# Kernel optimization log

Measured on AMD Instinct MI355X. Metric: run time of the kernel, lower is better.

The kernel has to match this reference:

```python
import jax, jax.numpy as jnp
import numpy as np
from math import sqrt

DIM = 256

def setup_inputs() -> dict:
    key = jax.random.key(0)
    k1, k2, k3, k4 = jax.random.split(key, 4)
    B, T, D, H, R = 2, 4096, DIM, 8, 32
    # xavier-uniform-ish scaled params
    def xavier(k, shape, fan_in, fan_out):
        a = sqrt(6.0 / (fan_in + fan_out))
        return jax.random.uniform(k, shape, jnp.float32, -a, a)
    x = jax.random.normal(k1, (B, T, D), jnp.float32)
    Q = xavier(k2, (H, R, D), D, R)
    K = xavier(k3, (H, R, D), D, R)
    VO = xavier(k4, (H, D, D), D, D)
    return {"x": x, "Q": Q, "K": K, "VO": VO}

def reference(x, Q, K, VO):
    # x: [b,t,d]; Q,K: [h,r,d]; VO: [h,d,e]
    d = x.shape[-1]
    q = jnp.einsum('btd,hrd->bhtr', x, Q)          # low-rank query proj
    k = jnp.einsum('bud,hrd->bhur', x, K)          # low-rank key proj
    scores = jnp.einsum('bhtr,bhur->bhtu', q, k) / sqrt(d)
    attn = jax.nn.softmax(scores, axis=-1)         # softmax over u (keys)
    ctx = jnp.einsum('bhtu,bud->bhtd', attn, x)    # values are raw x
    out = jnp.einsum('bhtd,hde->bte', ctx, VO)     # fused value-output proj, summed over heads
    return out
```

## Files before the change

### kernel.cpp

```cpp
#include <hip/hip_runtime.h>
#include <hip/hip_bf16.h>
#include <cstdint>
#include <cstddef>

typedef __attribute__((ext_vector_type(8))) __bf16 bf16x8;
typedef __attribute__((ext_vector_type(4))) float f32x4;
typedef __attribute__((ext_vector_type(16))) float f32x16;

#define MFMA16(a, b, c) __builtin_amdgcn_mfma_f32_16x16x32_bf16((a), (b), (c), 0, 0, 0)
#define MFMA32(a, b, c) __builtin_amdgcn_mfma_f32_32x32x16_bf16((a), (b), (c), 0, 0, 0)

__device__ __forceinline__ f32x16 zf16() {
    f32x16 z;
    #pragma unroll
    for (int r = 0; r < 16; ++r) z[r] = 0.f;
    return z;
}

__device__ __forceinline__ unsigned pk2(float lo, float hi) {
    unsigned w;
    asm("v_cvt_pk_bf16_f32 %0, %1, %2" : "=v"(w) : "v"(lo), "v"(hi));
    return w;
}
__device__ __forceinline__ void swap32(unsigned& a, unsigned& b) {
    asm("v_permlane32_swap_b32 %0, %1" : "+v"(a), "+v"(b));
}
__device__ __forceinline__ bf16x8 mkfrag(unsigned a, unsigned b, unsigned c, unsigned d) {
    union { unsigned u[4]; bf16x8 v; } x;
    x.u[0] = a; x.u[1] = b; x.u[2] = c; x.u[3] = d;
    return x.v;
}

__global__ __launch_bounds__(256) void prep(const float* __restrict__ x,
                                            const float* __restrict__ Qw,
                                            const float* __restrict__ Kw,
                                            const float* __restrict__ VO,
                                            __bf16* __restrict__ xT,
                                            __bf16* __restrict__ xrow,
                                            __bf16* __restrict__ wb,
                                            __bf16* __restrict__ vot) {
    __shared__ float tile[64][65];
    const int bid = blockIdx.x;
    if (bid < 512) {
        const int b = bid >> 8;
        const int rem = bid & 255;
        const int tt = rem >> 2, dd = rem & 3;
        const int t0 = tt * 64, d0 = dd * 64;
        #pragma unroll
        for (int j = 0; j < 16; ++j) {
            int idx = j * 256 + threadIdx.x;
            int t = idx >> 6, d = idx & 63;
            float v = x[((size_t)(b * 4096 + t0 + t)) * 256 + d0 + d];
            tile[t][d] = v;
            xrow[((size_t)(b * 4096 + t0 + t)) * 256 + d0 + d] = (__bf16)v;
        }
        __syncthreads();
        #pragma unroll
        for (int j = 0; j < 16; ++j) {
            int idx = j * 256 + threadIdx.x;
            int d = idx >> 6, t = idx & 63;
            xT[((size_t)(b * 256 + d0 + d)) * 4096 + t0 + t] = (__bf16)tile[t][d];
        }
    } else if (bid < 640) {
        const int k = bid - 512;
        const int h = k >> 4;
        const int rem = k & 15;
        const int dt = rem >> 2, et = rem & 3;
        const int d0 = dt * 64, e0 = et * 64;
        #pragma unroll
        for (int j = 0; j < 16; ++j) {
            int idx = j * 256 + threadIdx.x;
            int d = idx >> 6, e = idx & 63;
            tile[d][e] = VO[((size_t)(h * 256 + d0 + d)) * 256 + e0 + e];
        }
        __syncthreads();
        #pragma unroll
        for (int j = 0; j < 16; ++j) {
            int idx = j * 256 + threadIdx.x;
            int e = idx >> 6, d = idx & 63;
            vot[((size_t)(e0 + e)) * 2048 + h * 256 + d0 + d] = (__bf16)tile[d][e];
        }
    } else {
        const float cl = 1.4426950408889634f / 16.0f;
        #pragma unroll
        for (int e = 0; e < 2; ++e) {
            int i = (bid - 640) * 512 + e * 256 + threadIdx.x;
            float v = (i < 65536) ? Qw[i] * cl : Kw[i - 65536];
            wb[i] = (__bf16)v;
        }
    }
}

__global__ __launch_bounds__(256) void proj_kernel(const __bf16* __restrict__ xrow,
                                                   const __bf16* __restrict__ wb,
                                                   __bf16* __restrict__ qo,
                                                   __bf16* __restrict__ ko) {
    const int w = threadIdx.x >> 6;
    const int l = threadIdx.x & 63;
    const int g = l >> 4, c = l & 15;
    const int tg = blockIdx.x * 64 + w * 16;

    bf16x8 af[8];
    #pragma unroll
    for (int kk = 0; kk < 8; ++kk)
        af[kk] = *(const bf16x8*)(xrow + (size_t)(tg + c) * 256 + kk * 32 + g * 8);

    const int b = tg >> 12, t = tg & 4095;
    #pragma unroll
    for (int hs = 0; hs < 16; ++hs) {
        const int h = hs >> 1, s = hs & 1;
        const __bf16* W = wb + (size_t)(s * 8 + h) * 8192;
        f32x4 acc0 = {0.f, 0.f, 0.f, 0.f}, acc1 = {0.f, 0.f, 0.f, 0.f};
        #pragma unroll
        for (int kk = 0; kk < 8; ++kk) {
            bf16x8 b0 = *(const bf16x8*)(W + (size_t)c * 256 + kk * 32 + g * 8);
            bf16x8 b1 = *(const bf16x8*)(W + (size_t)(16 + c) * 256 + kk * 32 + g * 8);
            acc0 = MFMA16(af[kk], b0, acc0);
            acc1 = MFMA16(af[kk], b1, acc1);
        }
        __bf16* outp = s ? ko : qo;
        const size_t obase = (size_t)(b * 8 + h) * 4096 + t;
        #pragma unroll
        for (int i = 0; i < 4; ++i) {
            outp[(obase + 4 * g + i) * 32 + c]      = (__bf16)acc0[i];
            outp[(obase + 4 * g + i) * 32 + 16 + c] = (__bf16)acc1[i];
        }
    }
}

__device__ __forceinline__ void stage_x(const __bf16* __restrict__ xTg_b,
                                        unsigned char* xbuf, int u0, int tid) {
    #pragma unroll
    for (int j = 0; j < 4; ++j) {
        int ch = j * 512 + tid;
        int d = ch >> 3;
        int slog = (ch & 7) ^ (d & 7);
        const __bf16* src = xTg_b + (size_t)d * 4096 + u0 + slog * 8;
        unsigned char* dst = xbuf + (size_t)(j * 512 + (tid & ~63)) * 16;
        __builtin_amdgcn_global_load_lds(
            (const __attribute__((address_space(1))) unsigned int*)src,
            (__attribute__((address_space(3))) unsigned int*)dst, 16, 0, 0);
    }
}

#define MKFRAG(dst, V, base)                                   \
    {                                                          \
        unsigned wa = pk2(V[(base) + 0], V[(base) + 1]);       \
        unsigned wb_ = pk2(V[(base) + 2], V[(base) + 3]);      \
        unsigned wc = pk2(V[(base) + 4], V[(base) + 5]);       \
        unsigned wd = pk2(V[(base) + 6], V[(base) + 7]);       \
        swap32(wa, wc);                                        \
        swap32(wb_, wd);                                       \
        dst = mkfrag(wa, wb_, wc, wd);                         \
    }

__global__ __launch_bounds__(512, 2) void attn_kernel(const __bf16* __restrict__ qg,
                                                      const __bf16* __restrict__ kg,
                                                      const __bf16* __restrict__ xTg,
                                                      __bf16* __restrict__ ctx) {
    __shared__ __align__(16) unsigned char lds[65536 + 1024];
    unsigned char* xbuf0 = lds;
    unsigned char* xbuf1 = lds + 32768;

    const int bid = blockIdx.x;
    const int bh = bid >> 4;
    const int tt = bid & 15;
    const int b = bh >> 3, h = bh & 7;
    const int t0 = tt * 256;
    const int tid = threadIdx.x;
    const int w = tid >> 6;
    const int l = tid & 63;
    const int l31 = l & 31, hi = l >> 5;

    float* scale_w = (float*)(lds + 65536) + w * 32;

    const __bf16* xTg_b = xTg + (size_t)b * 256 * 4096;
    const __bf16* kg_bh = kg + (size_t)bh * 4096 * 32;

    const size_t qoff = ((size_t)bh * 4096 + t0 + w * 32 + l31) * 32;
    const bf16x8 qf0 = *(const bf16x8*)(qg + qoff + hi * 8);
    const bf16x8 qf1 = *(const bf16x8*)(qg + qoff + 16 + hi * 8);

    f32x16 acc[8];
    #pragma unroll
    for (int n = 0; n < 8; ++n)
        #pragma unroll
        for (int r = 0; r < 16; ++r) acc[n][r] = 0.f;

    float lsum = 0.f;
    const int swz = (l31 & 7) << 4;

    bf16x8 kA[2][2];
    #pragma unroll
    for (int s = 0; s < 2; ++s)
        #pragma unroll
        for (int st = 0; st < 2; ++st)
            kA[s][st] = *(const bf16x8*)(kg_bh + (size_t)(s * 32 + l31) * 32 + st * 16 + hi * 8);

    stage_x(xTg_b, xbuf0, 0, tid);
    __syncthreads();

    bf16x8 pf[4];
    for (int ut = 0; ut < 64; ++ut) {
        unsigned char* xcur = (ut & 1) ? xbuf1 : xbuf0;
        unsigned char* xnxt = (ut & 1) ? xbuf0 : xbuf1;
        if (ut < 63) stage_x(xTg_b, xnxt, (ut + 1) * 64, tid);

        f32x16 s0 = MFMA32(kA[0][0], qf0, zf16());
        s0 = MFMA32(kA[0][1], qf1, s0);
        f32x16 s1 = MFMA32(kA[1][0], qf0, zf16());
        s1 = MFMA32(kA[1][1], qf1, s1);

        if (ut < 63) {
            const __bf16* kp = kg_bh + (size_t)(ut + 1) * 64 * 32;
            #pragma unroll
            for (int s = 0; s < 2; ++s)
                #pragma unroll
                for (int st = 0; st < 2; ++st)
                    kA[s][st] = *(const bf16x8*)(kp + (size_t)(s * 32 + l31) * 32 + st * 16 + hi * 8);
        }

        float rs = 0.f;
        #pragma unroll
        for (int r = 0; r < 16; ++r) {
            float p = __builtin_amdgcn_exp2f(s0[r]);
            s0[r] = p; rs += p;
        }
        #pragma unroll
        for (int r = 0; r < 16; ++r) {
            float p = __builtin_amdgcn_exp2f(s1[r]);
            s1[r] = p; rs += p;
        }
        lsum += rs;

        bf16x8 pf0, pf1, pf2, pf3;
        MKFRAG(pf0, s0, 0);
        MKFRAG(pf1, s0, 8);
        MKFRAG(pf2, s1, 0);
        MKFRAG(pf3, s1, 8);
        pf[0] = pf0; pf[1] = pf1; pf[2] = pf2; pf[3] = pf3;

        __builtin_amdgcn_s_setprio(1);
        #pragma unroll
        for (int kk = 0; kk < 4; ++kk) {
            #pragma unroll
            for (int n = 0; n < 8; ++n) {
                const bf16x8 xb = *(const bf16x8*)(xcur + (n * 32 + l31) * 128 +
                                                   ((kk * 32 + hi * 16) ^ swz));
                acc[n] = MFMA32(pf[kk], xb, acc[n]);
            }
        }
        __builtin_amdgcn_s_setprio(0);

        asm volatile("s_waitcnt vmcnt(4)" ::: "memory");
        __builtin_amdgcn_s_barrier();
    }

    lsum += __shfl_xor(lsum, 32);
    const float linv = 1.0f / lsum;
    if (!hi) scale_w[l31] = linv;
    f32x4 iv[4];
    #pragma unroll
    for (int q4 = 0; q4 < 4; ++q4)
        iv[q4] = *(const f32x4*)&scale_w[q4 * 8 + hi * 4];
    #pragma unroll
    for (int n = 0; n < 8; ++n) {
        #pragma unroll
        for (int r = 0; r < 16; ++r) {
            int t = t0 + w * 32 + (r & 3) + 8 * (r >> 2) + 4 * hi;
            int d = n * 32 + l31;
            ctx[((size_t)(b * 4096 + t) * 8 + h) * 256 + d] =
                (__bf16)(acc[n][r] * iv[r >> 2][r & 3]);
        }
    }
}

__global__ __launch_bounds__(256) void gemm_out(const __bf16* __restrict__ ctx,
                                                const __bf16* __restrict__ vot,
                                                float* __restrict__ out) {
    const int bid = blockIdx.x;
    const int mt2 = bid >> 1;
    const int eh = bid & 1;
    const int w = threadIdx.x >> 6;
    const int l = threadIdx.x & 63;
    const int l31 = l & 31, hi = l >> 5;
    const size_t a0row = (size_t)(mt2 * 64 + l31) * 2048;
    const size_t a1row = (size_t)(mt2 * 64 + 32 + l31) * 2048;
    const size_t brow  = (size_t)(eh * 128 + w * 32 + l31) * 2048;
    f32x16 acc0 = zf16(), acc1 = zf16();
    #pragma unroll 4
    for (int kk = 0; kk < 128; ++kk) {
        bf16x8 bfr = *(const bf16x8*)(vot + brow + kk * 16 + hi * 8);
        bf16x8 a0  = *(const bf16x8*)(ctx + a0row + kk * 16 + hi * 8);
        bf16x8 a1  = *(const bf16x8*)(ctx + a1row + kk * 16 + hi * 8);
        acc0 = MFMA32(a0, bfr, acc0);
        acc1 = MFMA32(a1, bfr, acc1);
    }
    const int e = eh * 128 + w * 32 + l31;
    #pragma unroll
    for (int r = 0; r < 16; ++r) {
        int crow = (r & 3) + 8 * (r >> 2) + 4 * hi;
        out[(size_t)(mt2 * 64 + crow) * 256 + e]      = acc0[r];
        out[(size_t)(mt2 * 64 + 32 + crow) * 256 + e] = acc1[r];
    }
}

extern "C" void kernel_launch(void* const* d_in, const int* in_sizes, int n_in,
                              void* d_out, int out_size, void* d_ws, size_t ws_size,
                              hipStream_t stream) {
    const float* x  = (const float*)d_in[0];
    const float* Qw = (const float*)d_in[1];
    const float* Kw = (const float*)d_in[2];
    const float* VO = (const float*)d_in[3];
    float* out = (float*)d_out;

    char* ws = (char*)d_ws;
    __bf16* xT   = (__bf16*)(ws);
    __bf16* xrow = (__bf16*)(ws + ((size_t)4 << 20));
    __bf16* qb   = (__bf16*)(ws + ((size_t)8 << 20));
    __bf16* kb   = (__bf16*)(ws + ((size_t)12 << 20));
    __bf16* wb   = (__bf16*)(ws + ((size_t)16 << 20));
    __bf16* vot  = (__bf16*)(ws + ((size_t)17 << 20));
    __bf16* ctx  = (__bf16*)(ws + ((size_t)18 << 20));

    prep<<<896, 256, 0, stream>>>(x, Qw, Kw, VO, xT, xrow, wb, vot);
    proj_kernel<<<128, 256, 0, stream>>>(xrow, wb, qb, kb);
    attn_kernel<<<256, 512, 0, stream>>>(qb, kb, xT, ctx);
    gemm_out<<<256, 256, 0, stream>>>(ctx, vot, out);
}
```

Baseline: 242.9 us.

## Split attention warps into 64-query by 128-dim tiles to halve LDS reads

Each warp now owns 64 queries and half of the 256 value dimensions, where before it owned 32 queries and all 256 dimensions. Every x fragment read from LDS now feeds two MFMAs (one per 32-query half), which halves LDS read traffic per MFMA in the PV product. The cost is that each warp computes twice as many QK scores and exponentials, so QK^T and exp work is duplicated across the two warps sharing a query group. Register use per warp stays about the same.

```diff
diff --git a/kernel.cpp b/kernel.cpp
--- a/kernel.cpp
+++ b/kernel.cpp
@@ -158,7 +158,7 @@
                                                       const __bf16* __restrict__ kg,
                                                       const __bf16* __restrict__ xTg,
                                                       __bf16* __restrict__ ctx) {
-    __shared__ __align__(16) unsigned char lds[65536 + 1024];
+    __shared__ __align__(16) unsigned char lds[65536 + 2048];
     unsigned char* xbuf0 = lds;
     unsigned char* xbuf1 = lds + 32768;
 
@@ -169,25 +169,32 @@
     const int t0 = tt * 256;
     const int tid = threadIdx.x;
     const int w = tid >> 6;
+    const int qgi = w >> 1;
+    const int dh = w & 1;
     const int l = tid & 63;
     const int l31 = l & 31, hi = l >> 5;
 
-    float* scale_w = (float*)(lds + 65536) + w * 32;
+    float* scale_w = (float*)(lds + 65536) + w * 64;
 
     const __bf16* xTg_b = xTg + (size_t)b * 256 * 4096;
     const __bf16* kg_bh = kg + (size_t)bh * 4096 * 32;
 
-    const size_t qoff = ((size_t)bh * 4096 + t0 + w * 32 + l31) * 32;
-    const bf16x8 qf0 = *(const bf16x8*)(qg + qoff + hi * 8);
-    const bf16x8 qf1 = *(const bf16x8*)(qg + qoff + 16 + hi * 8);
-
-    f32x16 acc[8];
-    #pragma unroll
-    for (int n = 0; n < 8; ++n)
-        #pragma unroll
-        for (int r = 0; r < 16; ++r) acc[n][r] = 0.f;
-
-    float lsum = 0.f;
+    bf16x8 qf[2][2];
+    #pragma unroll
+    for (int qh = 0; qh < 2; ++qh) {
+        const size_t qoff = ((size_t)bh * 4096 + t0 + qgi * 64 + qh * 32 + l31) * 32;
+        qf[qh][0] = *(const bf16x8*)(qg + qoff + hi * 8);
+        qf[qh][1] = *(const bf16x8*)(qg + qoff + 16 + hi * 8);
+    }
+
+    f32x16 acc[2][4];
+    #pragma unroll
+    for (int qh = 0; qh < 2; ++qh)
+        #pragma unroll
+        for (int n = 0; n < 4; ++n)
+            acc[qh][n] = zf16();
+
+    float lsum0 = 0.f, lsum1 = 0.f;
     const int swz = (l31 & 7) << 4;
 
     bf16x8 kA[2][2];
@@ -200,16 +207,19 @@
     stage_x(xTg_b, xbuf0, 0, tid);
     __syncthreads();
 
-    bf16x8 pf[4];
     for (int ut = 0; ut < 64; ++ut) {
         unsigned char* xcur = (ut & 1) ? xbuf1 : xbuf0;
         unsigned char* xnxt = (ut & 1) ? xbuf0 : xbuf1;
         if (ut < 63) stage_x(xTg_b, xnxt, (ut + 1) * 64, tid);
 
-        f32x16 s0 = MFMA32(kA[0][0], qf0, zf16());
-        s0 = MFMA32(kA[0][1], qf1, s0);
-        f32x16 s1 = MFMA32(kA[1][0], qf0, zf16());
-        s1 = MFMA32(kA[1][1], qf1, s1);
+        f32x16 s00 = MFMA32(kA[0][0], qf[0][0], zf16());
+        s00 = MFMA32(kA[0][1], qf[0][1], s00);
+        f32x16 s01 = MFMA32(kA[1][0], qf[0][0], zf16());
+        s01 = MFMA32(kA[1][1], qf[0][1], s01);
+        f32x16 s10 = MFMA32(kA[0][0], qf[1][0], zf16());
+        s10 = MFMA32(kA[0][1], qf[1][1], s10);
+        f32x16 s11 = MFMA32(kA[1][0], qf[1][0], zf16());
+        s11 = MFMA32(kA[1][1], qf[1][1], s11);
 
         if (ut < 63) {
             const __bf16* kp = kg_bh + (size_t)(ut + 1) * 64 * 32;
@@ -220,34 +230,37 @@
                     kA[s][st] = *(const bf16x8*)(kp + (size_t)(s * 32 + l31) * 32 + st * 16 + hi * 8);
         }
 
-        float rs = 0.f;
+        float rs0 = 0.f, rs1 = 0.f;
         #pragma unroll
         for (int r = 0; r < 16; ++r) {
-            float p = __builtin_amdgcn_exp2f(s0[r]);
-            s0[r] = p; rs += p;
-        }
-        #pragma unroll
-        for (int r = 0; r < 16; ++r) {
-            float p = __builtin_amdgcn_exp2f(s1[r]);
-            s1[r] = p; rs += p;
-        }
-        lsum += rs;
-
-        bf16x8 pf0, pf1, pf2, pf3;
-        MKFRAG(pf0, s0, 0);
-        MKFRAG(pf1, s0, 8);
-        MKFRAG(pf2, s1, 0);
-        MKFRAG(pf3, s1, 8);
-        pf[0] = pf0; pf[1] = pf1; pf[2] = pf2; pf[3] = pf3;
+            float p;
+            p = __builtin_amdgcn_exp2f(s00[r]); s00[r] = p; rs0 += p;
+            p = __builtin_amdgcn_exp2f(s01[r]); s01[r] = p; rs0 += p;
+            p = __builtin_amdgcn_exp2f(s10[r]); s10[r] = p; rs1 += p;
+            p = __builtin_amdgcn_exp2f(s11[r]); s11[r] = p; rs1 += p;
+        }
+        lsum0 += rs0;
+        lsum1 += rs1;
+
+        bf16x8 pf0[4], pf1[4];
+        MKFRAG(pf0[0], s00, 0);
+        MKFRAG(pf0[1], s00, 8);
+        MKFRAG(pf0[2], s01, 0);
+        MKFRAG(pf0[3], s01, 8);
+        MKFRAG(pf1[0], s10, 0);
+        MKFRAG(pf1[1], s10, 8);
+        MKFRAG(pf1[2], s11, 0);
+        MKFRAG(pf1[3], s11, 8);
 
         __builtin_amdgcn_s_setprio(1);
         #pragma unroll
         for (int kk = 0; kk < 4; ++kk) {
             #pragma unroll
-            for (int n = 0; n < 8; ++n) {
-                const bf16x8 xb = *(const bf16x8*)(xcur + (n * 32 + l31) * 128 +
-                                                   ((kk * 32 + hi * 16) ^ swz));
-                acc[n] = MFMA32(pf[kk], xb, acc[n]);
+            for (int n = 0; n < 4; ++n) {
+                const bf16x8 xb = *(const bf16x8*)(xcur +
+                    (dh * 128 + n * 32 + l31) * 128 + ((kk * 32 + hi * 16) ^ swz));
+                acc[0][n] = MFMA32(pf0[kk], xb, acc[0][n]);
+                acc[1][n] = MFMA32(pf1[kk], xb, acc[1][n]);
             }
         }
         __builtin_amdgcn_s_setprio(0);
@@ -256,21 +269,27 @@
         __builtin_amdgcn_s_barrier();
     }
 
-    lsum += __shfl_xor(lsum, 32);
-    const float linv = 1.0f / lsum;
-    if (!hi) scale_w[l31] = linv;
-    f32x4 iv[4];
-    #pragma unroll
-    for (int q4 = 0; q4 < 4; ++q4)
-        iv[q4] = *(const f32x4*)&scale_w[q4 * 8 + hi * 4];
-    #pragma unroll
-    for (int n = 0; n < 8; ++n) {
-        #pragma unroll
-        for (int r = 0; r < 16; ++r) {
-            int t = t0 + w * 32 + (r & 3) + 8 * (r >> 2) + 4 * hi;
-            int d = n * 32 + l31;
-            ctx[((size_t)(b * 4096 + t) * 8 + h) * 256 + d] =
-                (__bf16)(acc[n][r] * iv[r >> 2][r & 3]);
+    lsum0 += __shfl_xor(lsum0, 32);
+    lsum1 += __shfl_xor(lsum1, 32);
+    if (!hi) {
+        scale_w[l31]      = 1.0f / lsum0;
+        scale_w[32 + l31] = 1.0f / lsum1;
+    }
+    #pragma unroll
+    for (int qh = 0; qh < 2; ++qh) {
+        f32x4 iv[4];
+        #pragma unroll
+        for (int q4 = 0; q4 < 4; ++q4)
+            iv[q4] = *(const f32x4*)&scale_w[qh * 32 + q4 * 8 + hi * 4];
+        #pragma unroll
+        for (int n = 0; n < 4; ++n) {
+            #pragma unroll
+            for (int r = 0; r < 16; ++r) {
+                int t = t0 + qgi * 64 + qh * 32 + (r & 3) + 8 * (r >> 2) + 4 * hi;
+                int d = dh * 128 + n * 32 + l31;
+                ctx[((size_t)(b * 4096 + t) * 8 + h) * 256 + d] =
+                    (__bf16)(acc[qh][n][r] * iv[r >> 2][r & 3]);
+            }
         }
     }
 }
```

Result: slower. 285.0 us (+17.4%).

## Switch attention P·V to FP8 MFMA with FP8-transposed x and register-staged LDS

Applied to the files above, without the earlier changes.

The transposed copy of x is now stored as FP8 instead of bf16, and the softmax probabilities are packed to FP8 so the P·V product uses the 32x32x16 FP8 MFMA. The aim is to halve the bytes of x read per tile and to use the faster FP8 matrix path. The direct global-to-LDS async loads are replaced by register loads written into a padded LDS layout (72-byte rows, no XOR swizzle) followed by a full __syncthreads. This risks accuracy loss from FP8 rounding of both x and the probabilities, and may stall more on the register-staged prefetch.

```diff
diff --git a/kernel.cpp b/kernel.cpp
--- a/kernel.cpp
+++ b/kernel.cpp
@@ -9,6 +9,7 @@
 
 #define MFMA16(a, b, c) __builtin_amdgcn_mfma_f32_16x16x32_bf16((a), (b), (c), 0, 0, 0)
 #define MFMA32(a, b, c) __builtin_amdgcn_mfma_f32_32x32x16_bf16((a), (b), (c), 0, 0, 0)
+#define MFMA8(a, b, c)  __builtin_amdgcn_mfma_f32_32x32x16_fp8_fp8((a), (b), (c), 0, 0, 0)
 
 __device__ __forceinline__ f32x16 zf16() {
     f32x16 z;
@@ -17,25 +18,15 @@
     return z;
 }
 
-__device__ __forceinline__ unsigned pk2(float lo, float hi) {
-    unsigned w;
-    asm("v_cvt_pk_bf16_f32 %0, %1, %2" : "=v"(w) : "v"(lo), "v"(hi));
-    return w;
-}
 __device__ __forceinline__ void swap32(unsigned& a, unsigned& b) {
     asm("v_permlane32_swap_b32 %0, %1" : "+v"(a), "+v"(b));
-}
-__device__ __forceinline__ bf16x8 mkfrag(unsigned a, unsigned b, unsigned c, unsigned d) {
-    union { unsigned u[4]; bf16x8 v; } x;
-    x.u[0] = a; x.u[1] = b; x.u[2] = c; x.u[3] = d;
-    return x.v;
 }
 
 __global__ __launch_bounds__(256) void prep(const float* __restrict__ x,
                                             const float* __restrict__ Qw,
                                             const float* __restrict__ Kw,
                                             const float* __restrict__ VO,
-                                            __bf16* __restrict__ xT,
+                                            unsigned char* __restrict__ x8T,
                                             __bf16* __restrict__ xrow,
                                             __bf16* __restrict__ wb,
                                             __bf16* __restrict__ vot) {
@@ -56,10 +47,14 @@
         }
         __syncthreads();
         #pragma unroll
-        for (int j = 0; j < 16; ++j) {
+        for (int j = 0; j < 8; ++j) {
             int idx = j * 256 + threadIdx.x;
-            int d = idx >> 6, t = idx & 63;
-            xT[((size_t)(b * 256 + d0 + d)) * 4096 + t0 + t] = (__bf16)tile[t][d];
+            int d = idx >> 5, tp = idx & 31;
+            float v0 = tile[tp * 2][d];
+            float v1 = tile[tp * 2 + 1][d];
+            int wpk = __builtin_amdgcn_cvt_pk_fp8_f32(v0, v1, 0, false);
+            *(unsigned short*)(x8T + (size_t)(b * 256 + d0 + d) * 4096 + t0 + tp * 2) =
+                (unsigned short)wpk;
         }
     } else if (bid < 640) {
         const int k = bid - 512;
@@ -128,39 +123,28 @@
     }
 }
 
-__device__ __forceinline__ void stage_x(const __bf16* __restrict__ xTg_b,
-                                        unsigned char* xbuf, int u0, int tid) {
-    #pragma unroll
-    for (int j = 0; j < 4; ++j) {
-        int ch = j * 512 + tid;
-        int d = ch >> 3;
-        int slog = (ch & 7) ^ (d & 7);
-        const __bf16* src = xTg_b + (size_t)d * 4096 + u0 + slog * 8;
-        unsigned char* dst = xbuf + (size_t)(j * 512 + (tid & ~63)) * 16;
-        __builtin_amdgcn_global_load_lds(
-            (const __attribute__((address_space(1))) unsigned int*)src,
-            (__attribute__((address_space(3))) unsigned int*)dst, 16, 0, 0);
-    }
-}
-
-#define MKFRAG(dst, V, base)                                   \
-    {                                                          \
-        unsigned wa = pk2(V[(base) + 0], V[(base) + 1]);       \
-        unsigned wb_ = pk2(V[(base) + 2], V[(base) + 3]);      \
-        unsigned wc = pk2(V[(base) + 4], V[(base) + 5]);       \
-        unsigned wd = pk2(V[(base) + 6], V[(base) + 7]);       \
-        swap32(wa, wc);                                        \
-        swap32(wb_, wd);                                       \
-        dst = mkfrag(wa, wb_, wc, wd);                         \
+
+#define MK8FRAG(dst, V, base)                                                  \
+    {                                                                          \
+        unsigned d0 = 0, d1 = 0;                                               \
+        d0 = __builtin_amdgcn_cvt_pk_fp8_f32(V[(base) + 0], V[(base) + 1], d0, false); \
+        d0 = __builtin_amdgcn_cvt_pk_fp8_f32(V[(base) + 2], V[(base) + 3], d0, true);  \
+        d1 = __builtin_amdgcn_cvt_pk_fp8_f32(V[(base) + 4], V[(base) + 5], d1, false); \
+        d1 = __builtin_amdgcn_cvt_pk_fp8_f32(V[(base) + 6], V[(base) + 7], d1, true);  \
+        swap32(d0, d1);                                                        \
+        union { unsigned u[2]; long l; } z;                                    \
+        z.u[0] = d0; z.u[1] = d1;                                              \
+        dst = z.l;                                                             \
     }
 
 __global__ __launch_bounds__(512, 2) void attn_kernel(const __bf16* __restrict__ qg,
                                                       const __bf16* __restrict__ kg,
-                                                      const __bf16* __restrict__ xTg,
+                                                      const unsigned char* __restrict__ x8g,
                                                       __bf16* __restrict__ ctx) {
-    __shared__ __align__(16) unsigned char lds[65536 + 1024];
+    __shared__ __align__(16) unsigned char lds[2 * 18432 + 1024];
     unsigned char* xbuf0 = lds;
-    unsigned char* xbuf1 = lds + 32768;
+    unsigned char* xbuf1 = lds + 18432;
+    float* scale_base = (float*)(lds + 36864);
 
     const int bid = blockIdx.x;
     const int bh = bid >> 4;
@@ -172,10 +156,13 @@
     const int l = tid & 63;
     const int l31 = l & 31, hi = l >> 5;
 
-    float* scale_w = (float*)(lds + 65536) + w * 32;
-
-    const __bf16* xTg_b = xTg + (size_t)b * 256 * 4096;
+    float* scale_w = scale_base + w * 32;
+
+    const unsigned char* x8b = x8g + (size_t)b * 256 * 4096;
     const __bf16* kg_bh = kg + (size_t)bh * 4096 * 32;
+
+    const int srow = tid >> 1;
+    const int soff = (tid & 1) * 32;
 
     const size_t qoff = ((size_t)bh * 4096 + t0 + w * 32 + l31) * 32;
     const bf16x8 qf0 = *(const bf16x8*)(qg + qoff + hi * 8);
@@ -188,7 +175,6 @@
         for (int r = 0; r < 16; ++r) acc[n][r] = 0.f;
 
     float lsum = 0.f;
-    const int swz = (l31 & 7) << 4;
 
     bf16x8 kA[2][2];
     #pragma unroll
@@ -197,14 +183,28 @@
         for (int st = 0; st < 2; ++st)
             kA[s][st] = *(const bf16x8*)(kg_bh + (size_t)(s * 32 + l31) * 32 + st * 16 + hi * 8);
 
-    stage_x(xTg_b, xbuf0, 0, tid);
+    {
+        const unsigned char* sp = x8b + (size_t)srow * 4096 + soff;
+        uint4 la = *(const uint4*)sp;
+        uint4 lb = *(const uint4*)(sp + 16);
+        unsigned char* dp = xbuf0 + srow * 72 + soff;
+        union { uint4 v; unsigned long long q[2]; } ua, ub;
+        ua.v = la; ub.v = lb;
+        ((unsigned long long*)dp)[0] = ua.q[0];
+        ((unsigned long long*)dp)[1] = ua.q[1];
+        ((unsigned long long*)(dp + 16))[0] = ub.q[0];
+        ((unsigned long long*)(dp + 16))[1] = ub.q[1];
+    }
     __syncthreads();
 
-    bf16x8 pf[4];
     for (int ut = 0; ut < 64; ++ut) {
         unsigned char* xcur = (ut & 1) ? xbuf1 : xbuf0;
         unsigned char* xnxt = (ut & 1) ? xbuf0 : xbuf1;
-        if (ut < 63) stage_x(xTg_b, xnxt, (ut + 1) * 64, tid);
+
+        const int u_next = ((ut + 1) & 63) * 64;
+        const unsigned char* sp = x8b + (size_t)srow * 4096 + u_next + soff;
+        const uint4 la = *(const uint4*)sp;
+        const uint4 lb = *(const uint4*)(sp + 16);
 
         f32x16 s0 = MFMA32(kA[0][0], qf0, zf16());
         s0 = MFMA32(kA[0][1], qf1, s0);
@@ -233,27 +233,34 @@
         }
         lsum += rs;
 
-        bf16x8 pf0, pf1, pf2, pf3;
-        MKFRAG(pf0, s0, 0);
-        MKFRAG(pf1, s0, 8);
-        MKFRAG(pf2, s1, 0);
-        MKFRAG(pf3, s1, 8);
-        pf[0] = pf0; pf[1] = pf1; pf[2] = pf2; pf[3] = pf3;
+        long pf0, pf1, pf2, pf3;
+        MK8FRAG(pf0, s0, 0);
+        MK8FRAG(pf1, s0, 8);
+        MK8FRAG(pf2, s1, 0);
+        MK8FRAG(pf3, s1, 8);
 
         __builtin_amdgcn_s_setprio(1);
         #pragma unroll
         for (int kk = 0; kk < 4; ++kk) {
+            const long pa = (kk == 0) ? pf0 : (kk == 1) ? pf1 : (kk == 2) ? pf2 : pf3;
             #pragma unroll
             for (int n = 0; n < 8; ++n) {
-                const bf16x8 xb = *(const bf16x8*)(xcur + (n * 32 + l31) * 128 +
-                                                   ((kk * 32 + hi * 16) ^ swz));
-                acc[n] = MFMA32(pf[kk], xb, acc[n]);
+                const long xb = *(const long*)(xcur + (n * 32 + l31) * 72 + kk * 16 + hi * 8);
+                acc[n] = MFMA8(pa, xb, acc[n]);
             }
         }
         __builtin_amdgcn_s_setprio(0);
 
-        asm volatile("s_waitcnt vmcnt(4)" ::: "memory");
-        __builtin_amdgcn_s_barrier();
+        {
+            unsigned char* dp = xnxt + srow * 72 + soff;
+            union { uint4 v; unsigned long long q[2]; } ua, ub;
+            ua.v = la; ub.v = lb;
+            ((unsigned long long*)dp)[0] = ua.q[0];
+            ((unsigned long long*)dp)[1] = ua.q[1];
+            ((unsigned long long*)(dp + 16))[0] = ub.q[0];
+            ((unsigned long long*)(dp + 16))[1] = ub.q[1];
+        }
+        __syncthreads();
     }
 
     lsum += __shfl_xor(lsum, 32);
@@ -315,7 +322,7 @@
     float* out = (float*)d_out;
 
     char* ws = (char*)d_ws;
-    __bf16* xT   = (__bf16*)(ws);
+    unsigned char* x8 = (unsigned char*)(ws);
     __bf16* xrow = (__bf16*)(ws + ((size_t)4 << 20));
     __bf16* qb   = (__bf16*)(ws + ((size_t)8 << 20));
     __bf16* kb   = (__bf16*)(ws + ((size_t)12 << 20));
@@ -323,8 +330,8 @@
     __bf16* vot  = (__bf16*)(ws + ((size_t)17 << 20));
     __bf16* ctx  = (__bf16*)(ws + ((size_t)18 << 20));
 
-    prep<<<896, 256, 0, stream>>>(x, Qw, Kw, VO, xT, xrow, wb, vot);
+    prep<<<896, 256, 0, stream>>>(x, Qw, Kw, VO, x8, xrow, wb, vot);
     proj_kernel<<<128, 256, 0, stream>>>(xrow, wb, qb, kb);
-    attn_kernel<<<256, 512, 0, stream>>>(qb, kb, xT, ctx);
+    attn_kernel<<<256, 512, 0, stream>>>(qb, kb, x8, ctx);
     gemm_out<<<256, 256, 0, stream>>>(ctx, vot, out);
 }
```

New measurement: 213.5 us (median of 3 runs). 12.1% less time.
